# Optimization experiments

Hardware: AMD Instinct MI355X
Metric: run time of the kernel (lower is better)

## Reference

```python
import jax, jax.numpy as jnp
import numpy as np

N_NODES = 100000
N_EDGES = 1600000
N_GRAPHS = 1024
F = 128
L = 3  # num_gnn_layers
EPS = 1e-5


def _ln(x, g, b):
    mu = jnp.mean(x, axis=-1, keepdims=True)
    v = jnp.mean((x - mu) ** 2, axis=-1, keepdims=True)
    return (x - mu) * jax.lax.rsqrt(v + EPS) * g + b


def setup_inputs() -> dict:
    key = jax.random.key(0)
    ks = jax.random.split(key, 40)
    s = 0.05
    d = {}
    d['x'] = jax.random.normal(ks[0], (N_NODES, F), jnp.float32)
    d['w'] = jax.random.uniform(ks[1], (N_NODES, 1), jnp.float32)
    d['edge_index'] = jax.random.randint(ks[2], (2, N_EDGES), 0, N_NODES)
    d['batch'] = jnp.sort(jax.random.randint(ks[3], (N_NODES,), 0, N_GRAPHS))
    # input linear: (monomer_features+1) -> gc_features
    d['W_in'] = jax.random.normal(ks[4], (F + 1, F), jnp.float32) * s
    d['b_in'] = jnp.zeros((F,), jnp.float32)
    # stacked GCBlock params [L, ...]
    d['sage_Wl'] = jax.random.normal(ks[5], (L, F, F), jnp.float32) * s
    d['sage_bl'] = jnp.zeros((L, F), jnp.float32)
    d['sage_Wr'] = jax.random.normal(ks[6], (L, F, F), jnp.float32) * s
    d['ln1_g'] = jnp.ones((L, F), jnp.float32)
    d['ln1_b'] = jnp.zeros((L, F), jnp.float32)
    d['lin1_W'] = jax.random.normal(ks[7], (L, F, F), jnp.float32) * s
    d['lin1_b'] = jnp.zeros((L, F), jnp.float32)
    d['lin2_W'] = jax.random.normal(ks[8], (L, F, F), jnp.float32) * s
    d['lin2_b'] = jnp.zeros((L, F), jnp.float32)
    d['ln2_g'] = jnp.ones((L, F), jnp.float32)
    d['ln2_b'] = jnp.zeros((L, F), jnp.float32)
    # MeanDiffFeatureBlock: Linear(2F -> F)
    d['mdf_W'] = jax.random.normal(ks[9], (2 * F, F), jnp.float32) * s
    d['mdf_b'] = jnp.zeros((F,), jnp.float32)
    # mean PoolingLayer params
    d['pln1_g'] = jnp.ones((F,), jnp.float32)
    d['pln1_b'] = jnp.zeros((F,), jnp.float32)
    d['plin1_W'] = jax.random.normal(ks[10], (F, F), jnp.float32) * s
    d['plin1_b'] = jnp.zeros((F,), jnp.float32)
    d['plin2_W'] = jax.random.normal(ks[11], (F, F), jnp.float32) * s
    d['plin2_b'] = jnp.zeros((F,), jnp.float32)
    d['pln2_g'] = jnp.ones((F,), jnp.float32)
    d['pln2_b'] = jnp.zeros((F,), jnp.float32)
    return d


def reference(x, w, edge_index, batch, W_in, b_in, sage_Wl, sage_bl, sage_Wr,
              ln1_g, ln1_b, lin1_W, lin1_b, lin2_W, lin2_b, ln2_g, ln2_b,
              mdf_W, mdf_b, pln1_g, pln1_b, plin1_W, plin1_b, plin2_W, plin2_b,
              pln2_g, pln2_b):
    src, dst = edge_index[0], edge_index[1]
    # in-degree for SAGE mean aggregation (clamped so isolated nodes -> 0 agg)
    deg = jax.ops.segment_sum(jnp.ones((N_EDGES,), jnp.float32), dst,
                              num_segments=N_NODES)
    deg = jnp.maximum(deg, 1.0)[:, None]
    # graph sizes for global_mean_pool
    cnt = jax.ops.segment_sum(jnp.ones((N_NODES,), jnp.float32), batch,
                              num_segments=N_GRAPHS)
    cnt = jnp.maximum(cnt, 1.0)[:, None]

    # inilinear on [x, weight-fraction]  (scalers are identity at init)
    h = jnp.concatenate([x, w], axis=-1) @ W_in + b_in  # [N, F]

    def gc_block(h, p):
        Wl, bl, Wr, g1, b1, W1, bb1, W2, bb2, g2, b2 = p
        # SAGEConv: lin_l(mean_j x_j) + lin_r(x_i)
        agg = jax.ops.segment_sum(h[src], dst, num_segments=N_NODES) / deg
        y = agg @ Wl + bl + h @ Wr
        y1 = _ln(y + h, g1, b1)
        y2 = jax.nn.elu(y1 @ W1 + bb1) @ W2 + bb2  # dropout = identity (eval)
        return _ln(y2 + y1, g2, b2), None

    h, _ = jax.lax.scan(gc_block, h,
                        (sage_Wl, sage_bl, sage_Wr, ln1_g, ln1_b,
                         lin1_W, lin1_b, lin2_W, lin2_b, ln2_g, ln2_b))

    # MeanDiffFeatureBlock
    gm = jax.ops.segment_sum(h, batch, num_segments=N_GRAPHS) / cnt  # [B, F]
    h = jnp.concatenate([h, h - gm[batch]], axis=-1) @ mdf_W + mdf_b

    # mean PoolingLayer
    p = jax.ops.segment_sum(h, batch, num_segments=N_GRAPHS) / cnt  # [B, F]
    hh = _ln(p, pln1_g, pln1_b)
    y = jax.nn.elu(hh @ plin1_W + plin1_b) @ plin2_W + plin2_b
    return _ln(y + hh, pln2_g, pln2_b)  # [B, F]
```

## Files before the change

kernel.cpp:

```cpp
#include <hip/hip_runtime.h>
#include <math.h>

#define NN 100000
#define NE 1600000
#define NG 1024
#define FF 128
#define BSH 9
#define NBK ((NN + 511) >> BSH)
#define RB 256
#define BCAP 16384

typedef __attribute__((ext_vector_type(8))) short short8;
typedef __attribute__((ext_vector_type(4))) float f32x4;
typedef __attribute__((ext_vector_type(2))) float f32x2;

__device__ __forceinline__ unsigned short f2b(float f) {
    union { float f; unsigned u; } v; v.f = f;
    unsigned r = (v.u + 0x7FFF + ((v.u >> 16) & 1)) >> 16;
    return (unsigned short)r;
}
__device__ __forceinline__ float us2f(unsigned short u) {
    union { unsigned u; float f; } v; v.u = ((unsigned)u) << 16; return v.f;
}
__device__ __forceinline__ float fast_elu(float v) {
    float e = __builtin_amdgcn_exp2f(v * 1.44269504088896340736f) - 1.0f;
    return v > 0.f ? v : e;
}
__device__ __forceinline__ uint2 pk8(const float* v) {
    unsigned lo = 0, hi = 0;
    lo = (unsigned)__builtin_amdgcn_cvt_pk_fp8_f32(v[0], v[1], (int)lo, false);
    lo = (unsigned)__builtin_amdgcn_cvt_pk_fp8_f32(v[2], v[3], (int)lo, true);
    hi = (unsigned)__builtin_amdgcn_cvt_pk_fp8_f32(v[4], v[5], (int)hi, false);
    hi = (unsigned)__builtin_amdgcn_cvt_pk_fp8_f32(v[6], v[7], (int)hi, true);
    uint2 r; r.x = lo; r.y = hi; return r;
}

__global__ void init_bcur(int* __restrict__ bcur) {
    int b = blockIdx.x * blockDim.x + threadIdx.x;
    if (b < NBK) bcur[b] = b * BCAP;
}

__global__ __launch_bounds__(256)
void radix_scatter(const int* __restrict__ src, const int* __restrict__ dst,
                   int* __restrict__ bcur, unsigned* __restrict__ pairs, int n) {
    __shared__ int base[NBK];
    __shared__ int cnt[NBK];
    for (int i = threadIdx.x; i < NBK; i += 256) cnt[i] = 0;
    __syncthreads();
    const int per = (n + RB - 1) / RB;
    const int beg = blockIdx.x * per;
    const int end = min(n, beg + per);
    for (int i = beg + threadIdx.x; i < end; i += 256)
        atomicAdd(&cnt[dst[i] >> BSH], 1);
    __syncthreads();
    for (int i = threadIdx.x; i < NBK; i += 256)
        base[i] = cnt[i] ? atomicAdd(&bcur[i], cnt[i]) : 0;
    __syncthreads();
    for (int i = beg + threadIdx.x; i < end; i += 256) {
        int d = dst[i];
        int p = atomicAdd(&base[d >> BSH], 1);
        pairs[p] = ((unsigned)src[i] << BSH) | (unsigned)(d & 511);
    }
}

__global__ __launch_bounds__(256)
void bucket_build(const unsigned* __restrict__ pairs, const int* __restrict__ bcur,
                  int* __restrict__ row_beg, int* __restrict__ row_end,
                  float* __restrict__ inv_deg, int* __restrict__ ssrc) {
    __shared__ int cnt[512];
    __shared__ int curs[512];
    __shared__ int wsum[4];
    const int b = blockIdx.x;
    const int n0 = b << BSH;
    const int t = threadIdx.x;
    const int lane = t & 63, wid = t >> 6;

    for (int i = t; i < 512; i += 256) cnt[i] = 0;
    __syncthreads();
    const int beg = b * BCAP, end = bcur[b];
    for (int i = beg + t; i < end; i += 256)
        atomicAdd(&cnt[pairs[i] & 511], 1);
    __syncthreads();

    int c0 = cnt[2 * t], c1 = cnt[2 * t + 1];
    int v = c0 + c1;
    int x = v;
    #pragma unroll
    for (int o = 1; o < 64; o <<= 1) {
        int y = __shfl_up(x, o);
        if (lane >= o) x += y;
    }
    if (lane == 63) wsum[wid] = x;
    __syncthreads();
    if (t == 0) {
        int s = 0;
        #pragma unroll
        for (int w2 = 0; w2 < 4; ++w2) { int tv = wsum[w2]; wsum[w2] = s; s += tv; }
    }
    __syncthreads();
    int g0 = beg + wsum[wid] + x - v;
    int g1 = g0 + c0;
    curs[2 * t] = g0;
    curs[2 * t + 1] = g1;
    {
        int node = n0 + 2 * t;
        if (node < NN) {
            row_beg[node] = g0; row_end[node] = g1;
            inv_deg[node] = 1.0f / (float)(c0 > 1 ? c0 : 1);
        }
        node = n0 + 2 * t + 1;
        if (node < NN) {
            row_beg[node] = g1; row_end[node] = g1 + c1;
            inv_deg[node] = 1.0f / (float)(c1 > 1 ? c1 : 1);
        }
    }
    __syncthreads();
    for (int i = beg + t; i < end; i += 256) {
        unsigned pr = pairs[i];
        int p = atomicAdd(&curs[pr & 511], 1);
        ssrc[p] = (int)(pr >> BSH) << 7;
    }
}

__global__ __launch_bounds__(256)
void graph_offsets(const int* __restrict__ batch, int* __restrict__ g_off,
                   float* __restrict__ inv_cnt) {
    int g = blockIdx.x * blockDim.x + threadIdx.x;
    if (g > NG) return;
    if (g == NG) { g_off[NG] = NN; return; }
    int lo = 0, hi = NN;
    while (lo < hi) { int mid = (lo + hi) >> 1; if (batch[mid] < g) lo = mid + 1; else hi = mid; }
    int lo2 = lo, hi2 = NN;
    while (lo2 < hi2) { int mid = (lo2 + hi2) >> 1; if (batch[mid] < g + 1) lo2 = mid + 1; else hi2 = mid; }
    g_off[g] = lo;
    int c = lo2 - lo;
    inv_cnt[g] = 1.0f / (float)(c > 1 ? c : 1);
}

struct WTab { const float* a[16]; };
__global__ __launch_bounds__(256)
void prep_weights(WTab tab, unsigned short* __restrict__ dst) {
    int w = blockIdx.x >> 6;
    int idx = ((blockIdx.x & 63) << 8) + threadIdx.x;
    int j = idx & 7, lane = (idx >> 3) & 63, nt = (idx >> 9) & 7, kc = idx >> 12;
    int cb = lane & 15, rq = lane >> 4;
    int k = kc * 32 + rq * 8 + j;
    int n = nt * 16 + cb;
    dst[(size_t)w * 16384 + idx] = f2b(tab.a[w][k * 128 + n]);
}

__global__ __launch_bounds__(256)
void sage_agg(const unsigned char* __restrict__ h8, const int* __restrict__ row_beg,
              const int* __restrict__ row_end, const float* __restrict__ inv_deg,
              const int* __restrict__ ssrc, unsigned short* __restrict__ aggb) {
    const int wid = threadIdx.x >> 6;
    const int lane = threadIdx.x & 63;
    const int node = blockIdx.x * 4 + wid;
    const int eg = lane >> 4, j = lane & 15;
    const int jo = j * 8;
    const int beg = row_beg[node], end = row_end[node];
    f32x2 a0 = {0.f, 0.f}, a1 = {0.f, 0.f}, a2 = {0.f, 0.f}, a3 = {0.f, 0.f};
    for (int e = beg + eg; e < end; e += 32) {
        uint2 u[8];
        #pragma unroll
        for (int k = 0; k < 8; ++k) {
            int ek = e + 4 * k;
            bool ok = ek < end;
            int idx = ssrc[ok ? ek : e];
            uint2 uu = *(const uint2*)(h8 + (unsigned)(idx + jo));
            uu.x = ok ? uu.x : 0u;
            uu.y = ok ? uu.y : 0u;
            u[k] = uu;
        }
        #pragma unroll
        for (int k = 0; k < 8; ++k) {
            a0 += __builtin_amdgcn_cvt_pk_f32_fp8(u[k].x, false);
            a1 += __builtin_amdgcn_cvt_pk_f32_fp8(u[k].x, true);
            a2 += __builtin_amdgcn_cvt_pk_f32_fp8(u[k].y, false);
            a3 += __builtin_amdgcn_cvt_pk_f32_fp8(u[k].y, true);
        }
    }
    float af[8] = {a0.x, a0.y, a1.x, a1.y, a2.x, a2.y, a3.x, a3.y};
    #pragma unroll
    for (int k = 0; k < 8; ++k) {
        af[k] += __shfl_xor(af[k], 16);
        af[k] += __shfl_xor(af[k], 32);
    }
    if (eg == 0) {
        float id = inv_deg[node];
        #pragma unroll
        for (int nt = 0; nt < 8; ++nt)
            aggb[(size_t)node * 128 + nt * 16 + j] = f2b(af[nt] * id);
    }
}

__global__ __launch_bounds__(128)
void pool_mean_b(const unsigned short* __restrict__ src, const int* __restrict__ g_off,
                 const float* __restrict__ inv_cnt, float* __restrict__ out) {
    const int g = blockIdx.x;
    const int j = threadIdx.x;
    const int beg = g_off[g], end = g_off[g + 1];
    float s = 0.f;
    for (int n = beg; n < end; ++n) s += us2f(src[(size_t)n * FF + j]);
    out[(size_t)g * FF + j] = s * inv_cnt[g];
}

template<bool AB16, bool R1, int RESM, int ACT, bool LN, bool OF32, bool OB16, bool OB8>
__global__ __launch_bounds__(256)
void gemm_mfma(const void* __restrict__ A_,
               const unsigned short* __restrict__ Wf,
               const float* __restrict__ bias,
               const float* __restrict__ rvec, const float* __restrict__ rrow,
               const float* __restrict__ res,
               const float* __restrict__ lng, const float* __restrict__ lnb,
               float* __restrict__ outf, unsigned short* __restrict__ outb,
               unsigned char* __restrict__ outb8, int M) {
    __shared__ short Al[64 * 136];

    const int t = threadIdx.x;
    const int lane = t & 63, wid = t >> 6;
    const int m0 = blockIdx.x * 64;
    const int cb = lane & 15, rq = lane >> 4;

    if (AB16) {
        const unsigned short* Ab = (const unsigned short*)A_;
        for (int i = t; i < 1024; i += 256) {
            int row = i >> 4, seg = i & 15;
            int gr = m0 + row; if (gr >= M) gr = M - 1;
            *(uint4*)&Al[row * 136 + seg * 8] = *(const uint4*)&Ab[(size_t)gr * 128 + seg * 8];
        }
    } else {
        const float* Af = (const float*)A_;
        for (int i = t; i < 2048; i += 256) {
            int row = i >> 5, seg = i & 31;
            int gr = m0 + row; if (gr >= M) gr = M - 1;
            float4 v = *(const float4*)&Af[(size_t)gr * 128 + seg * 4];
            ushort4 o = {f2b(v.x), f2b(v.y), f2b(v.z), f2b(v.w)};
            *(ushort4*)&Al[row * 136 + seg * 4] = o;
        }
    }
    __syncthreads();

    f32x4 acc[8];
    #pragma unroll
    for (int nt = 0; nt < 8; ++nt) acc[nt] = (f32x4){0.f, 0.f, 0.f, 0.f};

    const int aoff_base = (wid * 16 + cb) * 136 + rq * 8;
    for (int kc = 0; kc < 4; ++kc) {
        short8 a0 = *(const short8*)&Al[aoff_base + kc * 32];
        #pragma unroll
        for (int nt = 0; nt < 8; ++nt) {
            short8 b0 = *(const short8*)&Wf[(size_t)(kc * 8 + nt) * 512 + lane * 8];
            acc[nt] = __builtin_amdgcn_mfma_f32_16x16x32_bf16(a0, b0, acc[nt], 0, 0, 0);
        }
    }

    float bs[8], rr[8], lg[8], lb[8];
    #pragma unroll
    for (int nt = 0; nt < 8; ++nt) {
        int col = nt * 16 + cb;
        bs[nt] = bias[col];
        if (R1) rr[nt] = rrow[col];
        if (LN) { lg[nt] = lng[col]; lb[nt] = lnb[col]; }
    }
    #pragma unroll
    for (int reg = 0; reg < 4; ++reg) {
        int m = m0 + wid * 16 + rq * 4 + reg;
        int mc = m < M ? m : M - 1;
        float v[8];
        #pragma unroll
        for (int nt = 0; nt < 8; ++nt) v[nt] = acc[nt][reg] + bs[nt];
        if (R1) {
            float rv = rvec[mc];
            #pragma unroll
            for (int nt = 0; nt < 8; ++nt) v[nt] += rv * rr[nt];
        }
        if (RESM == 1) {
            #pragma unroll
            for (int nt = 0; nt < 8; ++nt) v[nt] += res[(size_t)mc * 128 + nt * 16 + cb];
        }
        if (ACT == 1) {
            #pragma unroll
            for (int nt = 0; nt < 8; ++nt) v[nt] = fast_elu(v[nt]);
        }
        if (LN) {
            float s1 = 0.f, s2 = 0.f;
            #pragma unroll
            for (int nt = 0; nt < 8; ++nt) { s1 += v[nt]; s2 += v[nt] * v[nt]; }
            #pragma unroll
            for (int o = 8; o >= 1; o >>= 1) { s1 += __shfl_xor(s1, o); s2 += __shfl_xor(s2, o); }
            float mu = s1 * (1.f / 128.f);
            float rs = rsqrtf(s2 * (1.f / 128.f) - mu * mu + 1e-5f);
            #pragma unroll
            for (int nt = 0; nt < 8; ++nt) v[nt] = (v[nt] - mu) * rs * lg[nt] + lb[nt];
        }
        if (m < M) {
            #pragma unroll
            for (int nt = 0; nt < 8; ++nt) {
                size_t o = (size_t)m * 128 + nt * 16 + cb;
                if (OF32) outf[o] = v[nt];
                if (OB16) outb[o] = f2b(v[nt]);
            }
            if (OB8) *(uint2*)&outb8[(size_t)m * 128 + cb * 8] = pk8(v);
        }
    }
}

__global__ __launch_bounds__(256)
void gc_chain(const unsigned short* __restrict__ hin, const unsigned short* __restrict__ aggb,
              unsigned short* __restrict__ hout, unsigned char* __restrict__ h8out,
              const unsigned short* __restrict__ Wl_f, const unsigned short* __restrict__ Wr_f,
              const unsigned short* __restrict__ W1_f, const unsigned short* __restrict__ W2_f,
              const float* __restrict__ bl,
              const float* __restrict__ g1, const float* __restrict__ b1,
              const float* __restrict__ bb1, const float* __restrict__ bb2,
              const float* __restrict__ g2, const float* __restrict__ b2, int M) {
    __shared__ short Hl[64 * 136];
    __shared__ short Gl[64 * 136];

    const int t = threadIdx.x;
    const int lane = t & 63, wid = t >> 6;
    const int m0 = blockIdx.x * 64;
    const int cb = lane & 15, rq = lane >> 4;
    const int aoff_base = (wid * 16 + cb) * 136 + rq * 8;
    const int boff = lane * 8;

    for (int i = t; i < 1024; i += 256) {
        int row = i >> 4, seg = i & 15;
        int gr = m0 + row; if (gr >= M) gr = M - 1;
        *(uint4*)&Hl[row * 136 + seg * 8] = *(const uint4*)&hin[(size_t)gr * 128 + seg * 8];
        *(uint4*)&Gl[row * 136 + seg * 8] = *(const uint4*)&aggb[(size_t)gr * 128 + seg * 8];
    }
    __syncthreads();

    f32x4 acc[8];
    #pragma unroll
    for (int nt = 0; nt < 8; ++nt) acc[nt] = (f32x4){0.f, 0.f, 0.f, 0.f};

    for (int kc = 0; kc < 4; ++kc) {
        short8 a0 = *(const short8*)&Gl[aoff_base + kc * 32];
        short8 a1 = *(const short8*)&Hl[aoff_base + kc * 32];
        #pragma unroll
        for (int nt = 0; nt < 8; ++nt) {
            const size_t wo = (size_t)(kc * 8 + nt) * 512 + boff;
            acc[nt] = __builtin_amdgcn_mfma_f32_16x16x32_bf16(a0, *(const short8*)&Wl_f[wo], acc[nt], 0, 0, 0);
            acc[nt] = __builtin_amdgcn_mfma_f32_16x16x32_bf16(a1, *(const short8*)&Wr_f[wo], acc[nt], 0, 0, 0);
        }
    }

    float y1r[4][8];
    {
        float bs[8], lg[8], lb[8];
        #pragma unroll
        for (int nt = 0; nt < 8; ++nt) {
            int col = nt * 16 + cb;
            bs[nt] = bl[col]; lg[nt] = g1[col]; lb[nt] = b1[col];
        }
        #pragma unroll
        for (int reg = 0; reg < 4; ++reg) {
            int r = wid * 16 + rq * 4 + reg;
            float v[8];
            float s1 = 0.f, s2 = 0.f;
            #pragma unroll
            for (int nt = 0; nt < 8; ++nt) {
                v[nt] = acc[nt][reg] + bs[nt] + us2f((unsigned short)Hl[r * 136 + nt * 16 + cb]);
                s1 += v[nt]; s2 += v[nt] * v[nt];
            }
            #pragma unroll
            for (int o = 8; o >= 1; o >>= 1) { s1 += __shfl_xor(s1, o); s2 += __shfl_xor(s2, o); }
            float mu = s1 * (1.f / 128.f);
            float rs = rsqrtf(s2 * (1.f / 128.f) - mu * mu + 1e-5f);
            #pragma unroll
            for (int nt = 0; nt < 8; ++nt) {
                float y = (v[nt] - mu) * rs * lg[nt] + lb[nt];
                y1r[reg][nt] = y;
                Hl[r * 136 + nt * 16 + cb] = (short)f2b(y);
            }
        }
    }

    #pragma unroll
    for (int nt = 0; nt < 8; ++nt) acc[nt] = (f32x4){0.f, 0.f, 0.f, 0.f};
    for (int kc = 0; kc < 4; ++kc) {
        short8 a0 = *(const short8*)&Hl[aoff_base + kc * 32];
        #pragma unroll
        for (int nt = 0; nt < 8; ++nt)
            acc[nt] = __builtin_amdgcn_mfma_f32_16x16x32_bf16(
                a0, *(const short8*)&W1_f[(size_t)(kc * 8 + nt) * 512 + boff], acc[nt], 0, 0, 0);
    }
    {
        float bs[8];
        #pragma unroll
        for (int nt = 0; nt < 8; ++nt) bs[nt] = bb1[nt * 16 + cb];
        #pragma unroll
        for (int reg = 0; reg < 4; ++reg) {
            int r = wid * 16 + rq * 4 + reg;
            #pragma unroll
            for (int nt = 0; nt < 8; ++nt) {
                float v = fast_elu(acc[nt][reg] + bs[nt]);
                Gl[r * 136 + nt * 16 + cb] = (short)f2b(v);
            }
        }
    }

    #pragma unroll
    for (int nt = 0; nt < 8; ++nt) acc[nt] = (f32x4){0.f, 0.f, 0.f, 0.f};
    for (int kc = 0; kc < 4; ++kc) {
        short8 a0 = *(const short8*)&Gl[aoff_base + kc * 32];
        #pragma unroll
        for (int nt = 0; nt < 8; ++nt)
            acc[nt] = __builtin_amdgcn_mfma_f32_16x16x32_bf16(
                a0, *(const short8*)&W2_f[(size_t)(kc * 8 + nt) * 512 + boff], acc[nt], 0, 0, 0);
    }
    {
        float bs[8], lg[8], lb[8];
        #pragma unroll
        for (int nt = 0; nt < 8; ++nt) {
            int col = nt * 16 + cb;
            bs[nt] = bb2[col]; lg[nt] = g2[col]; lb[nt] = b2[col];
        }
        #pragma unroll
        for (int reg = 0; reg < 4; ++reg) {
            int r = wid * 16 + rq * 4 + reg;
            int m = m0 + r;
            float v[8];
            float s1 = 0.f, s2 = 0.f;
            #pragma unroll
            for (int nt = 0; nt < 8; ++nt) {
                v[nt] = acc[nt][reg] + bs[nt] + y1r[reg][nt];
                s1 += v[nt]; s2 += v[nt] * v[nt];
            }
            #pragma unroll
            for (int o = 8; o >= 1; o >>= 1) { s1 += __shfl_xor(s1, o); s2 += __shfl_xor(s2, o); }
            float mu = s1 * (1.f / 128.f);
            float rs = rsqrtf(s2 * (1.f / 128.f) - mu * mu + 1e-5f);
            if (m < M) {
                float fv[8];
                #pragma unroll
                for (int nt = 0; nt < 8; ++nt) {
                    fv[nt] = (v[nt] - mu) * rs * lg[nt] + lb[nt];
                    hout[(size_t)m * 128 + nt * 16 + cb] = f2b(fv[nt]);
                }
                *(uint2*)&h8out[(size_t)m * 128 + cb * 8] = pk8(fv);
            }
        }
    }
}

extern "C" void kernel_launch(void* const* d_in, const int* in_sizes, int n_in,
                              void* d_out, int out_size, void* d_ws, size_t ws_size,
                              hipStream_t stream) {
    const float* x      = (const float*)d_in[0];
    const float* w      = (const float*)d_in[1];
    const int*   ei     = (const int*)d_in[2];
    const int*   batch  = (const int*)d_in[3];
    const float* W_in   = (const float*)d_in[4];
    const float* b_in   = (const float*)d_in[5];
    const float* sage_Wl = (const float*)d_in[6];
    const float* sage_bl = (const float*)d_in[7];
    const float* sage_Wr = (const float*)d_in[8];
    const float* ln1_g  = (const float*)d_in[9];
    const float* ln1_b  = (const float*)d_in[10];
    const float* lin1_W = (const float*)d_in[11];
    const float* lin1_b = (const float*)d_in[12];
    const float* lin2_W = (const float*)d_in[13];
    const float* lin2_b = (const float*)d_in[14];
    const float* ln2_g  = (const float*)d_in[15];
    const float* ln2_b  = (const float*)d_in[16];
    const float* mdf_W  = (const float*)d_in[17];
    const float* mdf_b  = (const float*)d_in[18];
    const float* pln1_g = (const float*)d_in[19];
    const float* pln1_b = (const float*)d_in[20];
    const float* plin1_W = (const float*)d_in[21];
    const float* plin1_b = (const float*)d_in[22];
    const float* plin2_W = (const float*)d_in[23];
    const float* plin2_b = (const float*)d_in[24];
    const float* pln2_g = (const float*)d_in[25];
    const float* pln2_b = (const float*)d_in[26];
    float* out = (float*)d_out;

    const int* e_src = ei;
    const int* e_dst = ei + NE;

    float* ws = (float*)d_ws;
    size_t off = 0;
    float* gm    = ws + off; off += (size_t)NG * FF;
    float* hh    = ws + off; off += (size_t)NG * FF;
    float* tt    = ws + off; off += (size_t)NG * FF;
    float* inv_deg = ws + off; off += NN;
    float* inv_cnt = ws + off; off += NG;
    unsigned short* us = (unsigned short*)(ws + off);
    size_t uoff = 0;
    unsigned short* hb0  = us + uoff; uoff += (size_t)NN * FF;
    unsigned short* hb1  = us + uoff; uoff += (size_t)NN * FF;
    unsigned short* aggb = us + uoff; uoff += (size_t)NN * FF;
    unsigned short* wt   = us + uoff; uoff += (size_t)16 * 16384;
    int* iw = (int*)(us + uoff);
    size_t ioff = 0;
    unsigned* pairs = (unsigned*)iw; ioff += (size_t)NBK * BCAP;
    int* ssrc    = iw + ioff; ioff += (size_t)NBK * BCAP;
    int* row_beg = iw + ioff; ioff += NN;
    int* row_end = iw + ioff; ioff += NN;
    int* g_off   = iw + ioff; ioff += NG + 1;
    int* bcur    = iw + ioff; ioff += NBK;
    unsigned char* h8 = (unsigned char*)pairs;

    WTab tab;
    tab.a[0] = W_in;
    for (int l = 0; l < 3; ++l) {
        tab.a[1 + l]  = sage_Wl + (size_t)l * 16384;
        tab.a[4 + l]  = sage_Wr + (size_t)l * 16384;
        tab.a[7 + l]  = lin1_W + (size_t)l * 16384;
        tab.a[10 + l] = lin2_W + (size_t)l * 16384;
    }
    tab.a[13] = mdf_W;
    tab.a[14] = plin1_W;
    tab.a[15] = plin2_W;
    prep_weights<<<16 * 64, 256, 0, stream>>>(tab, wt);
    const unsigned short* win_t = wt + 0 * 16384;
    const unsigned short* wa_t  = wt + 13 * 16384;
    const unsigned short* p1_t  = wt + 14 * 16384;
    const unsigned short* p2_t  = wt + 15 * 16384;

    init_bcur<<<1, 256, 0, stream>>>(bcur);
    graph_offsets<<<(NG + 256) / 256, 256, 0, stream>>>(batch, g_off, inv_cnt);
    radix_scatter<<<RB, 256, 0, stream>>>(e_src, e_dst, bcur, pairs, NE);
    bucket_build<<<NBK, 256, 0, stream>>>(pairs, bcur, row_beg, row_end, inv_deg, ssrc);

    const int GN = (NN + 63) / 64;
    const int GB = NG / 64;

    gemm_mfma<false, true, 0, 0, false, false, true, true><<<GN, 256, 0, stream>>>(
        x, win_t, b_in, w, W_in + 128 * 128,
        nullptr, nullptr, nullptr, nullptr, hb0, h8, NN);

    unsigned short* hcur = hb0;
    unsigned short* hnxt = hb1;
    for (int l = 0; l < 3; ++l) {
        sage_agg<<<NN / 4, 256, 0, stream>>>(h8, row_beg, row_end, inv_deg, ssrc, aggb);
        gc_chain<<<GN, 256, 0, stream>>>(
            hcur, aggb, hnxt, h8,
            wt + (size_t)(1 + l) * 16384, wt + (size_t)(4 + l) * 16384,
            wt + (size_t)(7 + l) * 16384, wt + (size_t)(10 + l) * 16384,
            sage_bl + (size_t)l * FF,
            ln1_g + (size_t)l * FF, ln1_b + (size_t)l * FF,
            lin1_b + (size_t)l * FF, lin2_b + (size_t)l * FF,
            ln2_g + (size_t)l * FF, ln2_b + (size_t)l * FF, NN);
        unsigned short* tmp = hcur; hcur = hnxt; hnxt = tmp;
    }

    pool_mean_b<<<NG, 128, 0, stream>>>(hcur, g_off, inv_cnt, gm);
    gemm_mfma<false, false, 0, 0, true, true, false, false><<<GB, 256, 0, stream>>>(
        gm, wa_t, mdf_b, nullptr, nullptr,
        nullptr, pln1_g, pln1_b, hh, nullptr, nullptr, NG);
    gemm_mfma<false, false, 0, 1, false, true, false, false><<<GB, 256, 0, stream>>>(
        hh, p1_t, plin1_b, nullptr, nullptr,
        nullptr, nullptr, nullptr, tt, nullptr, nullptr, NG);
    gemm_mfma<false, false, 1, 0, true, true, false, false><<<GB, 256, 0, stream>>>(
        tt, p2_t, plin2_b, nullptr, nullptr,
        hh, pln2_g, pln2_b, out, nullptr, nullptr, NG);
}
```

Baseline: 563.0 us.

## Process two 16-row fragments per wave in gc_chain with 128-thread blocks

The gc_chain block shrinks from four waves to two, and each wave now computes 32 rows as two 16-row MFMA fragments. Every weight B-fragment loaded from global memory is reused across both fragments, halving weight fetch traffic per row. The cost is twice the accumulator registers, plus the y1r array growing to 2x4x8, which raises register pressure. Fewer waves per block could also reduce latency hiding.

New measurement: 588.3 us. +4.5%, slower.

```diff
diff --git a/kernel.cpp b/kernel.cpp
--- a/kernel.cpp
+++ b/kernel.cpp
@@ -306,7 +306,7 @@
     }
 }
 
-__global__ __launch_bounds__(256)
+__global__ __launch_bounds__(128, 2)
 void gc_chain(const unsigned short* __restrict__ hin, const unsigned short* __restrict__ aggb,
               unsigned short* __restrict__ hout, unsigned char* __restrict__ h8out,
               const unsigned short* __restrict__ Wl_f, const unsigned short* __restrict__ Wr_f,
@@ -322,10 +322,12 @@
     const int lane = t & 63, wid = t >> 6;
     const int m0 = blockIdx.x * 64;
     const int cb = lane & 15, rq = lane >> 4;
-    const int aoff_base = (wid * 16 + cb) * 136 + rq * 8;
+    const int r0 = wid * 32;
+    const int aoff0 = (r0 + cb) * 136 + rq * 8;
+    const int aoff1 = (r0 + 16 + cb) * 136 + rq * 8;
     const int boff = lane * 8;
 
-    for (int i = t; i < 1024; i += 256) {
+    for (int i = t; i < 1024; i += 128) {
         int row = i >> 4, seg = i & 15;
         int gr = m0 + row; if (gr >= M) gr = M - 1;
         *(uint4*)&Hl[row * 136 + seg * 8] = *(const uint4*)&hin[(size_t)gr * 128 + seg * 8];
@@ -333,22 +335,31 @@
     }
     __syncthreads();
 
-    f32x4 acc[8];
-    #pragma unroll
-    for (int nt = 0; nt < 8; ++nt) acc[nt] = (f32x4){0.f, 0.f, 0.f, 0.f};
+    f32x4 acc0[8], acc1[8];
+    #pragma unroll
+    for (int nt = 0; nt < 8; ++nt) {
+        acc0[nt] = (f32x4){0.f, 0.f, 0.f, 0.f};
+        acc1[nt] = (f32x4){0.f, 0.f, 0.f, 0.f};
+    }
 
     for (int kc = 0; kc < 4; ++kc) {
-        short8 a0 = *(const short8*)&Gl[aoff_base + kc * 32];
-        short8 a1 = *(const short8*)&Hl[aoff_base + kc * 32];
+        short8 ga = *(const short8*)&Gl[aoff0 + kc * 32];
+        short8 gb = *(const short8*)&Gl[aoff1 + kc * 32];
+        short8 ha = *(const short8*)&Hl[aoff0 + kc * 32];
+        short8 hb = *(const short8*)&Hl[aoff1 + kc * 32];
         #pragma unroll
         for (int nt = 0; nt < 8; ++nt) {
             const size_t wo = (size_t)(kc * 8 + nt) * 512 + boff;
-            acc[nt] = __builtin_amdgcn_mfma_f32_16x16x32_bf16(a0, *(const short8*)&Wl_f[wo], acc[nt], 0, 0, 0);
-            acc[nt] = __builtin_amdgcn_mfma_f32_16x16x32_bf16(a1, *(const short8*)&Wr_f[wo], acc[nt], 0, 0, 0);
-        }
-    }
-
-    float y1r[4][8];
+            short8 wl = *(const short8*)&Wl_f[wo];
+            short8 wr = *(const short8*)&Wr_f[wo];
+            acc0[nt] = __builtin_amdgcn_mfma_f32_16x16x32_bf16(ga, wl, acc0[nt], 0, 0, 0);
+            acc1[nt] = __builtin_amdgcn_mfma_f32_16x16x32_bf16(gb, wl, acc1[nt], 0, 0, 0);
+            acc0[nt] = __builtin_amdgcn_mfma_f32_16x16x32_bf16(ha, wr, acc0[nt], 0, 0, 0);
+            acc1[nt] = __builtin_amdgcn_mfma_f32_16x16x32_bf16(hb, wr, acc1[nt], 0, 0, 0);
+        }
+    }
+
+    float y1r[2][4][8];
     {
         float bs[8], lg[8], lb[8];
         #pragma unroll
@@ -357,60 +368,80 @@
             bs[nt] = bl[col]; lg[nt] = g1[col]; lb[nt] = b1[col];
         }
         #pragma unroll
-        for (int reg = 0; reg < 4; ++reg) {
-            int r = wid * 16 + rq * 4 + reg;
-            float v[8];
-            float s1 = 0.f, s2 = 0.f;
-            #pragma unroll
-            for (int nt = 0; nt < 8; ++nt) {
-                v[nt] = acc[nt][reg] + bs[nt] + us2f((unsigned short)Hl[r * 136 + nt * 16 + cb]);
-                s1 += v[nt]; s2 += v[nt] * v[nt];
+        for (int fr = 0; fr < 2; ++fr) {
+            #pragma unroll
+            for (int reg = 0; reg < 4; ++reg) {
+                int r = r0 + fr * 16 + rq * 4 + reg;
+                float v[8];
+                float s1 = 0.f, s2 = 0.f;
+                #pragma unroll
+                for (int nt = 0; nt < 8; ++nt) {
+                    float a = fr ? acc1[nt][reg] : acc0[nt][reg];
+                    v[nt] = a + bs[nt] + us2f((unsigned short)Hl[r * 136 + nt * 16 + cb]);
+                    s1 += v[nt]; s2 += v[nt] * v[nt];
+                }
+                #pragma unroll
+                for (int o = 8; o >= 1; o >>= 1) { s1 += __shfl_xor(s1, o); s2 += __shfl_xor(s2, o); }
+                float mu = s1 * (1.f / 128.f);
+                float rs = rsqrtf(s2 * (1.f / 128.f) - mu * mu + 1e-5f);
+                #pragma unroll
+                for (int nt = 0; nt < 8; ++nt) {
+                    float y = (v[nt] - mu) * rs * lg[nt] + lb[nt];
+                    y1r[fr][reg][nt] = y;
+                    Hl[r * 136 + nt * 16 + cb] = (short)f2b(y);
+                }
             }
-            #pragma unroll
-            for (int o = 8; o >= 1; o >>= 1) { s1 += __shfl_xor(s1, o); s2 += __shfl_xor(s2, o); }
-            float mu = s1 * (1.f / 128.f);
-            float rs = rsqrtf(s2 * (1.f / 128.f) - mu * mu + 1e-5f);
-            #pragma unroll
-            for (int nt = 0; nt < 8; ++nt) {
-                float y = (v[nt] - mu) * rs * lg[nt] + lb[nt];
-                y1r[reg][nt] = y;
-                Hl[r * 136 + nt * 16 + cb] = (short)f2b(y);
-            }
-        }
-    }
-
-    #pragma unroll
-    for (int nt = 0; nt < 8; ++nt) acc[nt] = (f32x4){0.f, 0.f, 0.f, 0.f};
+        }
+    }
+
+    #pragma unroll
+    for (int nt = 0; nt < 8; ++nt) {
+        acc0[nt] = (f32x4){0.f, 0.f, 0.f, 0.f};
+        acc1[nt] = (f32x4){0.f, 0.f, 0.f, 0.f};
+    }
     for (int kc = 0; kc < 4; ++kc) {
-        short8 a0 = *(const short8*)&Hl[aoff_base + kc * 32];
-        #pragma unroll
-        for (int nt = 0; nt < 8; ++nt)
-            acc[nt] = __builtin_amdgcn_mfma_f32_16x16x32_bf16(
-                a0, *(const short8*)&W1_f[(size_t)(kc * 8 + nt) * 512 + boff], acc[nt], 0, 0, 0);
+        short8 a0 = *(const short8*)&Hl[aoff0 + kc * 32];
+        short8 a1 = *(const short8*)&Hl[aoff1 + kc * 32];
+        #pragma unroll
+        for (int nt = 0; nt < 8; ++nt) {
+            short8 b0 = *(const short8*)&W1_f[(size_t)(kc * 8 + nt) * 512 + boff];
+            acc0[nt] = __builtin_amdgcn_mfma_f32_16x16x32_bf16(a0, b0, acc0[nt], 0, 0, 0);
+            acc1[nt] = __builtin_amdgcn_mfma_f32_16x16x32_bf16(a1, b0, acc1[nt], 0, 0, 0);
+        }
     }
     {
         float bs[8];
         #pragma unroll
         for (int nt = 0; nt < 8; ++nt) bs[nt] = bb1[nt * 16 + cb];
         #pragma unroll
-        for (int reg = 0; reg < 4; ++reg) {
-            int r = wid * 16 + rq * 4 + reg;
-            #pragma unroll
-            for (int nt = 0; nt < 8; ++nt) {
-                float v = fast_elu(acc[nt][reg] + bs[nt]);
-                Gl[r * 136 + nt * 16 + cb] = (short)f2b(v);
+        for (int fr = 0; fr < 2; ++fr) {
+            #pragma unroll
+            for (int reg = 0; reg < 4; ++reg) {
+                int r = r0 + fr * 16 + rq * 4 + reg;
+                #pragma unroll
+                for (int nt = 0; nt < 8; ++nt) {
+                    float a = fr ? acc1[nt][reg] : acc0[nt][reg];
+                    float v = fast_elu(a + bs[nt]);
+                    Gl[r * 136 + nt * 16 + cb] = (short)f2b(v);
+                }
             }
         }
     }
 
     #pragma unroll
-    for (int nt = 0; nt < 8; ++nt) acc[nt] = (f32x4){0.f, 0.f, 0.f, 0.f};
+    for (int nt = 0; nt < 8; ++nt) {
+        acc0[nt] = (f32x4){0.f, 0.f, 0.f, 0.f};
+        acc1[nt] = (f32x4){0.f, 0.f, 0.f, 0.f};
+    }
     for (int kc = 0; kc < 4; ++kc) {
-        short8 a0 = *(const short8*)&Gl[aoff_base + kc * 32];
-        #pragma unroll
-        for (int nt = 0; nt < 8; ++nt)
-            acc[nt] = __builtin_amdgcn_mfma_f32_16x16x32_bf16(
-                a0, *(const short8*)&W2_f[(size_t)(kc * 8 + nt) * 512 + boff], acc[nt], 0, 0, 0);
+        short8 a0 = *(const short8*)&Gl[aoff0 + kc * 32];
+        short8 a1 = *(const short8*)&Gl[aoff1 + kc * 32];
+        #pragma unroll
+        for (int nt = 0; nt < 8; ++nt) {
+            short8 b0 = *(const short8*)&W2_f[(size_t)(kc * 8 + nt) * 512 + boff];
+            acc0[nt] = __builtin_amdgcn_mfma_f32_16x16x32_bf16(a0, b0, acc0[nt], 0, 0, 0);
+            acc1[nt] = __builtin_amdgcn_mfma_f32_16x16x32_bf16(a1, b0, acc1[nt], 0, 0, 0);
+        }
     }
     {
         float bs[8], lg[8], lb[8];
@@ -420,28 +451,32 @@
             bs[nt] = bb2[col]; lg[nt] = g2[col]; lb[nt] = b2[col];
         }
         #pragma unroll
-        for (int reg = 0; reg < 4; ++reg) {
-            int r = wid * 16 + rq * 4 + reg;
-            int m = m0 + r;
-            float v[8];
-            float s1 = 0.f, s2 = 0.f;
-            #pragma unroll
-            for (int nt = 0; nt < 8; ++nt) {
-                v[nt] = acc[nt][reg] + bs[nt] + y1r[reg][nt];
-                s1 += v[nt]; s2 += v[nt] * v[nt];
-            }
-            #pragma unroll
-            for (int o = 8; o >= 1; o >>= 1) { s1 += __shfl_xor(s1, o); s2 += __shfl_xor(s2, o); }
-            float mu = s1 * (1.f / 128.f);
-            float rs = rsqrtf(s2 * (1.f / 128.f) - mu * mu + 1e-5f);
-            if (m < M) {
-                float fv[8];
+        for (int fr = 0; fr < 2; ++fr) {
+            #pragma unroll
+            for (int reg = 0; reg < 4; ++reg) {
+                int r = r0 + fr * 16 + rq * 4 + reg;
+                int m = m0 + r;
+                float v[8];
+                float s1 = 0.f, s2 = 0.f;
                 #pragma unroll
                 for (int nt = 0; nt < 8; ++nt) {
-                    fv[nt] = (v[nt] - mu) * rs * lg[nt] + lb[nt];
-                    hout[(size_t)m * 128 + nt * 16 + cb] = f2b(fv[nt]);
+                    float a = fr ? acc1[nt][reg] : acc0[nt][reg];
+                    v[nt] = a + bs[nt] + y1r[fr][reg][nt];
+                    s1 += v[nt]; s2 += v[nt] * v[nt];
                 }
-                *(uint2*)&h8out[(size_t)m * 128 + cb * 8] = pk8(fv);
+                #pragma unroll
+                for (int o = 8; o >= 1; o >>= 1) { s1 += __shfl_xor(s1, o); s2 += __shfl_xor(s2, o); }
+                float mu = s1 * (1.f / 128.f);
+                float rs = rsqrtf(s2 * (1.f / 128.f) - mu * mu + 1e-5f);
+                if (m < M) {
+                    float fv[8];
+                    #pragma unroll
+                    for (int nt = 0; nt < 8; ++nt) {
+                        fv[nt] = (v[nt] - mu) * rs * lg[nt] + lb[nt];
+                        hout[(size_t)m * 128 + nt * 16 + cb] = f2b(fv[nt]);
+                    }
+                    *(uint2*)&h8out[(size_t)m * 128 + cb * 8] = pk8(fv);
+                }
             }
         }
     }
@@ -538,7 +573,7 @@
     unsigned short* hnxt = hb1;
     for (int l = 0; l < 3; ++l) {
         sage_agg<<<NN / 4, 256, 0, stream>>>(h8, row_beg, row_end, inv_deg, ssrc, aggb);
-        gc_chain<<<GN, 256, 0, stream>>>(
+        gc_chain<<<GN, 128, 0, stream>>>(
             hcur, aggb, hnxt, h8,
             wt + (size_t)(1 + l) * 16384, wt + (size_t)(4 + l) * 16384,
             wt + (size_t)(7 + l) * 16384, wt + (size_t)(10 + l) * 16384,
```

## Fuse SAGE neighbor aggregation into gc_chain kernel with double-buffered fp8 features

Applied to the files above, without the earlier changes.

Removes the separate sage_agg kernel and does the fp8 gather-mean for each 64-row tile inside gc_chain, writing the aggregated rows straight into shared memory. This drops the bf16 aggregate round trip through global memory and one launch per layer. Because gc_chain now reads fp8 features of other nodes while also writing the next fp8 features, the fp8 buffer is double-buffered, reusing the aggb space. The risk is lower parallelism: one wave now handles 16 nodes one after another, which lowers memory-level parallelism for the gather phase and leaves the MFMA phase waiting on it.

New measurement: 736.0 us. 1.31x slower.

```diff
diff --git a/kernel.cpp b/kernel.cpp
--- a/kernel.cpp
+++ b/kernel.cpp
@@ -149,51 +149,6 @@
     dst[(size_t)w * 16384 + idx] = f2b(tab.a[w][k * 128 + n]);
 }
 
-__global__ __launch_bounds__(256)
-void sage_agg(const unsigned char* __restrict__ h8, const int* __restrict__ row_beg,
-              const int* __restrict__ row_end, const float* __restrict__ inv_deg,
-              const int* __restrict__ ssrc, unsigned short* __restrict__ aggb) {
-    const int wid = threadIdx.x >> 6;
-    const int lane = threadIdx.x & 63;
-    const int node = blockIdx.x * 4 + wid;
-    const int eg = lane >> 4, j = lane & 15;
-    const int jo = j * 8;
-    const int beg = row_beg[node], end = row_end[node];
-    f32x2 a0 = {0.f, 0.f}, a1 = {0.f, 0.f}, a2 = {0.f, 0.f}, a3 = {0.f, 0.f};
-    for (int e = beg + eg; e < end; e += 32) {
-        uint2 u[8];
-        #pragma unroll
-        for (int k = 0; k < 8; ++k) {
-            int ek = e + 4 * k;
-            bool ok = ek < end;
-            int idx = ssrc[ok ? ek : e];
-            uint2 uu = *(const uint2*)(h8 + (unsigned)(idx + jo));
-            uu.x = ok ? uu.x : 0u;
-            uu.y = ok ? uu.y : 0u;
-            u[k] = uu;
-        }
-        #pragma unroll
-        for (int k = 0; k < 8; ++k) {
-            a0 += __builtin_amdgcn_cvt_pk_f32_fp8(u[k].x, false);
-            a1 += __builtin_amdgcn_cvt_pk_f32_fp8(u[k].x, true);
-            a2 += __builtin_amdgcn_cvt_pk_f32_fp8(u[k].y, false);
-            a3 += __builtin_amdgcn_cvt_pk_f32_fp8(u[k].y, true);
-        }
-    }
-    float af[8] = {a0.x, a0.y, a1.x, a1.y, a2.x, a2.y, a3.x, a3.y};
-    #pragma unroll
-    for (int k = 0; k < 8; ++k) {
-        af[k] += __shfl_xor(af[k], 16);
-        af[k] += __shfl_xor(af[k], 32);
-    }
-    if (eg == 0) {
-        float id = inv_deg[node];
-        #pragma unroll
-        for (int nt = 0; nt < 8; ++nt)
-            aggb[(size_t)node * 128 + nt * 16 + j] = f2b(af[nt] * id);
-    }
-}
-
 __global__ __launch_bounds__(128)
 void pool_mean_b(const unsigned short* __restrict__ src, const int* __restrict__ g_off,
                  const float* __restrict__ inv_cnt, float* __restrict__ out) {
@@ -307,7 +262,10 @@
 }
 
 __global__ __launch_bounds__(256)
-void gc_chain(const unsigned short* __restrict__ hin, const unsigned short* __restrict__ aggb,
+void gc_chain(const unsigned short* __restrict__ hin,
+              const unsigned char* __restrict__ h8in,
+              const int* __restrict__ row_beg, const int* __restrict__ row_end,
+              const float* __restrict__ inv_deg, const int* __restrict__ ssrc,
               unsigned short* __restrict__ hout, unsigned char* __restrict__ h8out,
               const unsigned short* __restrict__ Wl_f, const unsigned short* __restrict__ Wr_f,
               const unsigned short* __restrict__ W1_f, const unsigned short* __restrict__ W2_f,
@@ -329,7 +287,48 @@
         int row = i >> 4, seg = i & 15;
         int gr = m0 + row; if (gr >= M) gr = M - 1;
         *(uint4*)&Hl[row * 136 + seg * 8] = *(const uint4*)&hin[(size_t)gr * 128 + seg * 8];
-        *(uint4*)&Gl[row * 136 + seg * 8] = *(const uint4*)&aggb[(size_t)gr * 128 + seg * 8];
+    }
+
+    {
+        const int eg = lane >> 4, j = lane & 15, jo = j * 8;
+        for (int nl = 0; nl < 16; ++nl) {
+            int row = wid * 16 + nl;
+            int node = m0 + row; if (node >= NN) node = NN - 1;
+            const int beg = row_beg[node], end = row_end[node];
+            f32x2 a0 = {0.f, 0.f}, a1 = {0.f, 0.f}, a2 = {0.f, 0.f}, a3 = {0.f, 0.f};
+            for (int e = beg + eg; e < end; e += 32) {
+                uint2 u[8];
+                #pragma unroll
+                for (int k = 0; k < 8; ++k) {
+                    int ek = e + 4 * k;
+                    bool ok = ek < end;
+                    int idx = ssrc[ok ? ek : e];
+                    uint2 uu = *(const uint2*)(h8in + (unsigned)(idx + jo));
+                    uu.x = ok ? uu.x : 0u;
+                    uu.y = ok ? uu.y : 0u;
+                    u[k] = uu;
+                }
+                #pragma unroll
+                for (int k = 0; k < 8; ++k) {
+                    a0 += __builtin_amdgcn_cvt_pk_f32_fp8(u[k].x, false);
+                    a1 += __builtin_amdgcn_cvt_pk_f32_fp8(u[k].x, true);
+                    a2 += __builtin_amdgcn_cvt_pk_f32_fp8(u[k].y, false);
+                    a3 += __builtin_amdgcn_cvt_pk_f32_fp8(u[k].y, true);
+                }
+            }
+            float af[8] = {a0.x, a0.y, a1.x, a1.y, a2.x, a2.y, a3.x, a3.y};
+            #pragma unroll
+            for (int k = 0; k < 8; ++k) {
+                af[k] += __shfl_xor(af[k], 16);
+                af[k] += __shfl_xor(af[k], 32);
+            }
+            if (eg == 0) {
+                float id = inv_deg[node];
+                #pragma unroll
+                for (int nt = 0; nt < 8; ++nt)
+                    Gl[row * 136 + nt * 16 + j] = (short)f2b(af[nt] * id);
+            }
+        }
     }
     __syncthreads();
 
@@ -503,7 +502,8 @@
     int* row_end = iw + ioff; ioff += NN;
     int* g_off   = iw + ioff; ioff += NG + 1;
     int* bcur    = iw + ioff; ioff += NBK;
-    unsigned char* h8 = (unsigned char*)pairs;
+    unsigned char* h8a = (unsigned char*)pairs;
+    unsigned char* h8b = (unsigned char*)aggb;
 
     WTab tab;
     tab.a[0] = W_in;
@@ -532,14 +532,16 @@
 
     gemm_mfma<false, true, 0, 0, false, false, true, true><<<GN, 256, 0, stream>>>(
         x, win_t, b_in, w, W_in + 128 * 128,
-        nullptr, nullptr, nullptr, nullptr, hb0, h8, NN);
+        nullptr, nullptr, nullptr, nullptr, hb0, h8a, NN);
 
     unsigned short* hcur = hb0;
     unsigned short* hnxt = hb1;
+    unsigned char* h8cur = h8a;
+    unsigned char* h8nxt = h8b;
     for (int l = 0; l < 3; ++l) {
-        sage_agg<<<NN / 4, 256, 0, stream>>>(h8, row_beg, row_end, inv_deg, ssrc, aggb);
         gc_chain<<<GN, 256, 0, stream>>>(
-            hcur, aggb, hnxt, h8,
+            hcur, h8cur, row_beg, row_end, inv_deg, ssrc,
+            hnxt, h8nxt,
             wt + (size_t)(1 + l) * 16384, wt + (size_t)(4 + l) * 16384,
             wt + (size_t)(7 + l) * 16384, wt + (size_t)(10 + l) * 16384,
             sage_bl + (size_t)l * FF,
@@ -547,6 +549,7 @@
             lin1_b + (size_t)l * FF, lin2_b + (size_t)l * FF,
             ln2_g + (size_t)l * FF, ln2_b + (size_t)l * FF, NN);
         unsigned short* tmp = hcur; hcur = hnxt; hnxt = tmp;
+        unsigned char* t8 = h8cur; h8cur = h8nxt; h8nxt = t8;
     }
 
     pool_mean_b<<<NG, 128, 0, stream>>>(hcur, g_off, inv_cnt, gm);
```

## Make gc_chain persistent with LDS-resident weights and register prefetch of next tile

Applied to the files above, without the earlier changes.

gc_chain now launches 256 persistent blocks that each stage all four bf16 weight matrices (128 KB) into dynamic LDS once, then loop over 64-row node tiles. The A operands for h and agg are loaded straight into registers in MFMA fragment layout, and the next tile's rows are prefetched while the current tile computes. A single padded LDS tile replaces the two earlier ones. This removes repeated global/L2 weight reads per tile and overlaps input loads with compute, at the cost of one block per CU, lower occupancy and a large LDS footprint.

Measured after the change: 568.2 us. About the same (+0.9%).

```diff
diff --git a/kernel.cpp b/kernel.cpp
--- a/kernel.cpp
+++ b/kernel.cpp
@@ -9,6 +9,8 @@
 #define NBK ((NN + 511) >> BSH)
 #define RB 256
 #define BCAP 16384
+#define NPB 256
+#define GC_LDS ((4 * 16384 + 64 * 136) * 2)
 
 typedef __attribute__((ext_vector_type(8))) short short8;
 typedef __attribute__((ext_vector_type(4))) float f32x4;
@@ -34,6 +36,7 @@
     hi = (unsigned)__builtin_amdgcn_cvt_pk_fp8_f32(v[6], v[7], (int)hi, true);
     uint2 r; r.x = lo; r.y = hi; return r;
 }
+#define MFMA(a, b, c) __builtin_amdgcn_mfma_f32_16x16x32_bf16((a), (b), (c), 0, 0, 0)
 
 __global__ void init_bcur(int* __restrict__ bcur) {
     int b = blockIdx.x * blockDim.x + threadIdx.x;
@@ -251,7 +254,7 @@
         #pragma unroll
         for (int nt = 0; nt < 8; ++nt) {
             short8 b0 = *(const short8*)&Wf[(size_t)(kc * 8 + nt) * 512 + lane * 8];
-            acc[nt] = __builtin_amdgcn_mfma_f32_16x16x32_bf16(a0, b0, acc[nt], 0, 0, 0);
+            acc[nt] = MFMA(a0, b0, acc[nt]);
         }
     }
 
@@ -306,7 +309,7 @@
     }
 }
 
-__global__ __launch_bounds__(256)
+__global__ __launch_bounds__(256, 1)
 void gc_chain(const unsigned short* __restrict__ hin, const unsigned short* __restrict__ aggb,
               unsigned short* __restrict__ hout, unsigned char* __restrict__ h8out,
               const unsigned short* __restrict__ Wl_f, const unsigned short* __restrict__ Wr_f,
@@ -314,134 +317,182 @@
               const float* __restrict__ bl,
               const float* __restrict__ g1, const float* __restrict__ b1,
               const float* __restrict__ bb1, const float* __restrict__ bb2,
-              const float* __restrict__ g2, const float* __restrict__ b2, int M) {
-    __shared__ short Hl[64 * 136];
-    __shared__ short Gl[64 * 136];
+              const float* __restrict__ g2, const float* __restrict__ b2,
+              int M, int ntiles) {
+    extern __shared__ short smem[];
+    short* Wlds = smem;
+    short* Tl   = smem + 65536;
 
     const int t = threadIdx.x;
     const int lane = t & 63, wid = t >> 6;
-    const int m0 = blockIdx.x * 64;
     const int cb = lane & 15, rq = lane >> 4;
-    const int aoff_base = (wid * 16 + cb) * 136 + rq * 8;
+    const int band = wid * 16;
+    const int aoff_base = (band + cb) * 136 + rq * 8;
     const int boff = lane * 8;
-
-    for (int i = t; i < 1024; i += 256) {
-        int row = i >> 4, seg = i & 15;
-        int gr = m0 + row; if (gr >= M) gr = M - 1;
-        *(uint4*)&Hl[row * 136 + seg * 8] = *(const uint4*)&hin[(size_t)gr * 128 + seg * 8];
-        *(uint4*)&Gl[row * 136 + seg * 8] = *(const uint4*)&aggb[(size_t)gr * 128 + seg * 8];
-    }
-    __syncthreads();
-
-    f32x4 acc[8];
-    #pragma unroll
-    for (int nt = 0; nt < 8; ++nt) acc[nt] = (f32x4){0.f, 0.f, 0.f, 0.f};
-
-    for (int kc = 0; kc < 4; ++kc) {
-        short8 a0 = *(const short8*)&Gl[aoff_base + kc * 32];
-        short8 a1 = *(const short8*)&Hl[aoff_base + kc * 32];
-        #pragma unroll
-        for (int nt = 0; nt < 8; ++nt) {
-            const size_t wo = (size_t)(kc * 8 + nt) * 512 + boff;
-            acc[nt] = __builtin_amdgcn_mfma_f32_16x16x32_bf16(a0, *(const short8*)&Wl_f[wo], acc[nt], 0, 0, 0);
-            acc[nt] = __builtin_amdgcn_mfma_f32_16x16x32_bf16(a1, *(const short8*)&Wr_f[wo], acc[nt], 0, 0, 0);
-        }
-    }
-
-    float y1r[4][8];
+    const int fcol = rq * 8;
+
     {
-        float bs[8], lg[8], lb[8];
-        #pragma unroll
-        for (int nt = 0; nt < 8; ++nt) {
-            int col = nt * 16 + cb;
-            bs[nt] = bl[col]; lg[nt] = g1[col]; lb[nt] = b1[col];
-        }
-        #pragma unroll
-        for (int reg = 0; reg < 4; ++reg) {
-            int r = wid * 16 + rq * 4 + reg;
-            float v[8];
-            float s1 = 0.f, s2 = 0.f;
+        uint4* dst = (uint4*)Wlds;
+        const uint4* s0 = (const uint4*)Wl_f;
+        const uint4* s1 = (const uint4*)Wr_f;
+        const uint4* s2 = (const uint4*)W1_f;
+        const uint4* s3 = (const uint4*)W2_f;
+        for (int i = t; i < 2048; i += 256) {
+            dst[i]        = s0[i];
+            dst[2048 + i] = s1[i];
+            dst[4096 + i] = s2[i];
+            dst[6144 + i] = s3[i];
+        }
+    }
+    __syncthreads();
+
+    const short* WL  = Wlds;
+    const short* WR  = Wlds + 16384;
+    const short* W1m = Wlds + 32768;
+    const short* W2m = Wlds + 49152;
+
+    int tile = blockIdx.x;
+    short8 hp[4], gp[4];
+    {
+        int gr = tile * 64 + band + cb; if (gr >= M) gr = M - 1;
+        const unsigned short* hrow = hin  + (size_t)gr * 128 + fcol;
+        const unsigned short* grow = aggb + (size_t)gr * 128 + fcol;
+        #pragma unroll
+        for (int kc = 0; kc < 4; ++kc) {
+            hp[kc] = *(const short8*)(hrow + kc * 32);
+            gp[kc] = *(const short8*)(grow + kc * 32);
+        }
+    }
+
+    for (; tile < ntiles; tile += NPB) {
+        const int m0 = tile * 64;
+
+        #pragma unroll
+        for (int kc = 0; kc < 4; ++kc)
+            *(short8*)&Tl[aoff_base + kc * 32] = hp[kc];
+
+        f32x4 acc[8];
+        #pragma unroll
+        for (int nt = 0; nt < 8; ++nt) acc[nt] = (f32x4){0.f, 0.f, 0.f, 0.f};
+        #pragma unroll
+        for (int kc = 0; kc < 4; ++kc) {
             #pragma unroll
             for (int nt = 0; nt < 8; ++nt) {
-                v[nt] = acc[nt][reg] + bs[nt] + us2f((unsigned short)Hl[r * 136 + nt * 16 + cb]);
-                s1 += v[nt]; s2 += v[nt] * v[nt];
-            }
-            #pragma unroll
-            for (int o = 8; o >= 1; o >>= 1) { s1 += __shfl_xor(s1, o); s2 += __shfl_xor(s2, o); }
-            float mu = s1 * (1.f / 128.f);
-            float rs = rsqrtf(s2 * (1.f / 128.f) - mu * mu + 1e-5f);
+                const int wo = (kc * 8 + nt) * 512 + boff;
+                acc[nt] = MFMA(gp[kc], *(const short8*)&WL[wo], acc[nt]);
+                acc[nt] = MFMA(hp[kc], *(const short8*)&WR[wo], acc[nt]);
+            }
+        }
+
+        {
+            int tn = tile + NPB;
+            if (tn < ntiles) {
+                int gr = tn * 64 + band + cb; if (gr >= M) gr = M - 1;
+                const unsigned short* hrow = hin  + (size_t)gr * 128 + fcol;
+                const unsigned short* grow = aggb + (size_t)gr * 128 + fcol;
+                #pragma unroll
+                for (int kc = 0; kc < 4; ++kc) {
+                    hp[kc] = *(const short8*)(hrow + kc * 32);
+                    gp[kc] = *(const short8*)(grow + kc * 32);
+                }
+            }
+        }
+
+        float y1r[4][8];
+        {
+            float bs[8], lg[8], lb[8];
             #pragma unroll
             for (int nt = 0; nt < 8; ++nt) {
-                float y = (v[nt] - mu) * rs * lg[nt] + lb[nt];
-                y1r[reg][nt] = y;
-                Hl[r * 136 + nt * 16 + cb] = (short)f2b(y);
-            }
-        }
-    }
-
-    #pragma unroll
-    for (int nt = 0; nt < 8; ++nt) acc[nt] = (f32x4){0.f, 0.f, 0.f, 0.f};
-    for (int kc = 0; kc < 4; ++kc) {
-        short8 a0 = *(const short8*)&Hl[aoff_base + kc * 32];
-        #pragma unroll
-        for (int nt = 0; nt < 8; ++nt)
-            acc[nt] = __builtin_amdgcn_mfma_f32_16x16x32_bf16(
-                a0, *(const short8*)&W1_f[(size_t)(kc * 8 + nt) * 512 + boff], acc[nt], 0, 0, 0);
-    }
-    {
-        float bs[8];
-        #pragma unroll
-        for (int nt = 0; nt < 8; ++nt) bs[nt] = bb1[nt * 16 + cb];
-        #pragma unroll
-        for (int reg = 0; reg < 4; ++reg) {
-            int r = wid * 16 + rq * 4 + reg;
-            #pragma unroll
-            for (int nt = 0; nt < 8; ++nt) {
-                float v = fast_elu(acc[nt][reg] + bs[nt]);
-                Gl[r * 136 + nt * 16 + cb] = (short)f2b(v);
-            }
-        }
-    }
-
-    #pragma unroll
-    for (int nt = 0; nt < 8; ++nt) acc[nt] = (f32x4){0.f, 0.f, 0.f, 0.f};
-    for (int kc = 0; kc < 4; ++kc) {
-        short8 a0 = *(const short8*)&Gl[aoff_base + kc * 32];
-        #pragma unroll
-        for (int nt = 0; nt < 8; ++nt)
-            acc[nt] = __builtin_amdgcn_mfma_f32_16x16x32_bf16(
-                a0, *(const short8*)&W2_f[(size_t)(kc * 8 + nt) * 512 + boff], acc[nt], 0, 0, 0);
-    }
-    {
-        float bs[8], lg[8], lb[8];
-        #pragma unroll
-        for (int nt = 0; nt < 8; ++nt) {
-            int col = nt * 16 + cb;
-            bs[nt] = bb2[col]; lg[nt] = g2[col]; lb[nt] = b2[col];
-        }
-        #pragma unroll
-        for (int reg = 0; reg < 4; ++reg) {
-            int r = wid * 16 + rq * 4 + reg;
-            int m = m0 + r;
-            float v[8];
-            float s1 = 0.f, s2 = 0.f;
-            #pragma unroll
-            for (int nt = 0; nt < 8; ++nt) {
-                v[nt] = acc[nt][reg] + bs[nt] + y1r[reg][nt];
-                s1 += v[nt]; s2 += v[nt] * v[nt];
-            }
-            #pragma unroll
-            for (int o = 8; o >= 1; o >>= 1) { s1 += __shfl_xor(s1, o); s2 += __shfl_xor(s2, o); }
-            float mu = s1 * (1.f / 128.f);
-            float rs = rsqrtf(s2 * (1.f / 128.f) - mu * mu + 1e-5f);
-            if (m < M) {
-                float fv[8];
+                int col = nt * 16 + cb;
+                bs[nt] = bl[col]; lg[nt] = g1[col]; lb[nt] = b1[col];
+            }
+            #pragma unroll
+            for (int reg = 0; reg < 4; ++reg) {
+                int r = band + rq * 4 + reg;
+                float v[8];
+                float s1 = 0.f, s2 = 0.f;
                 #pragma unroll
                 for (int nt = 0; nt < 8; ++nt) {
-                    fv[nt] = (v[nt] - mu) * rs * lg[nt] + lb[nt];
-                    hout[(size_t)m * 128 + nt * 16 + cb] = f2b(fv[nt]);
+                    v[nt] = acc[nt][reg] + bs[nt] + us2f((unsigned short)Tl[r * 136 + nt * 16 + cb]);
+                    s1 += v[nt]; s2 += v[nt] * v[nt];
                 }
-                *(uint2*)&h8out[(size_t)m * 128 + cb * 8] = pk8(fv);
+                #pragma unroll
+                for (int o = 8; o >= 1; o >>= 1) { s1 += __shfl_xor(s1, o); s2 += __shfl_xor(s2, o); }
+                float mu = s1 * (1.f / 128.f);
+                float rs = rsqrtf(s2 * (1.f / 128.f) - mu * mu + 1e-5f);
+                #pragma unroll
+                for (int nt = 0; nt < 8; ++nt) {
+                    float y = (v[nt] - mu) * rs * lg[nt] + lb[nt];
+                    y1r[reg][nt] = y;
+                    Tl[r * 136 + nt * 16 + cb] = (short)f2b(y);
+                }
+            }
+        }
+
+        #pragma unroll
+        for (int nt = 0; nt < 8; ++nt) acc[nt] = (f32x4){0.f, 0.f, 0.f, 0.f};
+        #pragma unroll
+        for (int kc = 0; kc < 4; ++kc) {
+            short8 a0 = *(const short8*)&Tl[aoff_base + kc * 32];
+            #pragma unroll
+            for (int nt = 0; nt < 8; ++nt)
+                acc[nt] = MFMA(a0, *(const short8*)&W1m[(kc * 8 + nt) * 512 + boff], acc[nt]);
+        }
+        {
+            float bs[8];
+            #pragma unroll
+            for (int nt = 0; nt < 8; ++nt) bs[nt] = bb1[nt * 16 + cb];
+            #pragma unroll
+            for (int reg = 0; reg < 4; ++reg) {
+                int r = band + rq * 4 + reg;
+                #pragma unroll
+                for (int nt = 0; nt < 8; ++nt) {
+                    float v = fast_elu(acc[nt][reg] + bs[nt]);
+                    Tl[r * 136 + nt * 16 + cb] = (short)f2b(v);
+                }
+            }
+        }
+
+        #pragma unroll
+        for (int nt = 0; nt < 8; ++nt) acc[nt] = (f32x4){0.f, 0.f, 0.f, 0.f};
+        #pragma unroll
+        for (int kc = 0; kc < 4; ++kc) {
+            short8 a0 = *(const short8*)&Tl[aoff_base + kc * 32];
+            #pragma unroll
+            for (int nt = 0; nt < 8; ++nt)
+                acc[nt] = MFMA(a0, *(const short8*)&W2m[(kc * 8 + nt) * 512 + boff], acc[nt]);
+        }
+        {
+            float bs[8], lg[8], lb[8];
+            #pragma unroll
+            for (int nt = 0; nt < 8; ++nt) {
+                int col = nt * 16 + cb;
+                bs[nt] = bb2[col]; lg[nt] = g2[col]; lb[nt] = b2[col];
+            }
+            #pragma unroll
+            for (int reg = 0; reg < 4; ++reg) {
+                int r = band + rq * 4 + reg;
+                int m = m0 + r;
+                float v[8];
+                float s1 = 0.f, s2 = 0.f;
+                #pragma unroll
+                for (int nt = 0; nt < 8; ++nt) {
+                    v[nt] = acc[nt][reg] + bs[nt] + y1r[reg][nt];
+                    s1 += v[nt]; s2 += v[nt] * v[nt];
+                }
+                #pragma unroll
+                for (int o = 8; o >= 1; o >>= 1) { s1 += __shfl_xor(s1, o); s2 += __shfl_xor(s2, o); }
+                float mu = s1 * (1.f / 128.f);
+                float rs = rsqrtf(s2 * (1.f / 128.f) - mu * mu + 1e-5f);
+                if (m < M) {
+                    float fv[8];
+                    #pragma unroll
+                    for (int nt = 0; nt < 8; ++nt) {
+                        fv[nt] = (v[nt] - mu) * rs * lg[nt] + lb[nt];
+                        hout[(size_t)m * 128 + nt * 16 + cb] = f2b(fv[nt]);
+                    }
+                    *(uint2*)&h8out[(size_t)m * 128 + cb * 8] = pk8(fv);
+                }
             }
         }
     }
@@ -482,6 +533,13 @@
     const int* e_src = ei;
     const int* e_dst = ei + NE;
 
+    static bool attr_set = false;
+    if (!attr_set) {
+        (void)hipFuncSetAttribute(reinterpret_cast<const void*>(gc_chain),
+                                  hipFuncAttributeMaxDynamicSharedMemorySize, GC_LDS);
+        attr_set = true;
+    }
+
     float* ws = (float*)d_ws;
     size_t off = 0;
     float* gm    = ws + off; off += (size_t)NG * FF;
@@ -538,14 +596,14 @@
     unsigned short* hnxt = hb1;
     for (int l = 0; l < 3; ++l) {
         sage_agg<<<NN / 4, 256, 0, stream>>>(h8, row_beg, row_end, inv_deg, ssrc, aggb);
-        gc_chain<<<GN, 256, 0, stream>>>(
+        gc_chain<<<NPB, 256, GC_LDS, stream>>>(
             hcur, aggb, hnxt, h8,
             wt + (size_t)(1 + l) * 16384, wt + (size_t)(4 + l) * 16384,
             wt + (size_t)(7 + l) * 16384, wt + (size_t)(10 + l) * 16384,
             sage_bl + (size_t)l * FF,
             ln1_g + (size_t)l * FF, ln1_b + (size_t)l * FF,
             lin1_b + (size_t)l * FF, lin2_b + (size_t)l * FF,
-            ln2_g + (size_t)l * FF, ln2_b + (size_t)l * FF, NN);
+            ln2_g + (size_t)l * FF, ln2_b + (size_t)l * FF, NN, GN);
         unsigned short* tmp = hcur; hcur = hnxt; hnxt = tmp;
     }
 
```
